# Kernel tuning notes

Measured on AMD Instinct MI355X. Metric: run time of the kernel, lower is better.

## Reference

```python
import jax, jax.numpy as jnp
import numpy as np

B = 16
H, D, DV = 8, 64, 64
MAX_SEQLEN = 1024
ALPHA = 1.0


def setup_inputs() -> dict:
    key = jax.random.key(0)
    lengths = np.array([512 + (b * 97) % 513 for b in range(B)], dtype=np.int32)
    offsets = np.concatenate([[0], np.cumsum(lengths)]).astype(np.int32)  # (B+1,)
    T = int(offsets[-1])  # 12137
    k1, k2, k3 = jax.random.split(key, 3)
    tq = jax.random.normal(k1, (T, H * D), dtype=jnp.float32)
    tk = jax.random.normal(k2, (T, H * D), dtype=jnp.float32)
    tv = jax.random.normal(k3, (T, H * DV), dtype=jnp.float32)
    num_candidates = jnp.full((B,), 32, dtype=jnp.int32)
    num_contextuals = jnp.full((B,), 8, dtype=jnp.int32)
    return {
        "tq": tq, "tk": tk, "tv": tv,
        "offsets": jnp.asarray(offsets),
        "max_seqlen": MAX_SEQLEN,
        "num_candidates": num_candidates,
        "num_contextuals": num_contextuals,
    }


def _valid_attn_mask(N, lengths, num_candidates, num_contextuals):
    # HSTU mask: causal within history, contextual tokens act as position 0
    # (attend/attended bidirectionally w.r.t. history), targets (candidates)
    # attend to all history + themselves only (target_group_size == 1).
    ids = jnp.arange(N, dtype=jnp.int32)[None, :]              # (1, N)
    c = num_contextuals[:, None]                                # (B, 1)
    ids_adj = jnp.maximum(ids - c + 1, 0)                       # (B, N)
    max_ids = (lengths - num_contextuals + 1 - num_candidates)[:, None]  # (B, 1)
    ids_adj = jnp.minimum(ids_adj, max_ids)                     # all targets share id == max_ids
    row = ids_adj[:, :, None]                                   # (B, N, 1)
    col = ids_adj[:, None, :]                                   # (B, 1, N)
    dist = row - col
    eye = jnp.eye(N, dtype=bool)[None]
    valid = eye | (dist > 0)                                    # causal + self
    # contextual rows (adjusted id 0) attend all history (but not targets)
    valid = valid | ((row == 0) & (col < max_ids[:, :, None]))
    # mask out padding
    pad = jnp.arange(N, dtype=jnp.int32)[None, :] < lengths[:, None]  # (B, N)
    valid = valid & pad[:, :, None] & pad[:, None, :]
    return valid


def reference(tq, tk, tv, offsets, max_seqlen, num_candidates, num_contextuals):
    T = tq.shape[0]
    Bb = offsets.shape[0] - 1
    N = max_seqlen
    lengths = offsets[1:] - offsets[:-1]                        # (B,)
    # jagged -> padded dense via scatter
    t = jnp.arange(T, dtype=jnp.int32)
    b_idx = jnp.searchsorted(offsets, t, side="right").astype(jnp.int32) - 1
    n_idx = t - offsets[b_idx]
    q = jnp.zeros((Bb, N, H, D), tq.dtype).at[b_idx, n_idx].set(tq.reshape(T, H, D))
    k = jnp.zeros((Bb, N, H, D), tk.dtype).at[b_idx, n_idx].set(tk.reshape(T, H, D))
    v = jnp.zeros((Bb, N, H, DV), tv.dtype).at[b_idx, n_idx].set(tv.reshape(T, H, DV))
    valid = _valid_attn_mask(N, lengths, num_candidates, num_contextuals)  # (B, N, N)
    qk = jnp.einsum("bnhd,bmhd->bhnm", q, k) * ALPHA
    # HSTU non-softmax attention: silu(scores) / max_seqlen, masked
    attn = (jax.nn.silu(qk) / N) * valid[:, None, :, :].astype(qk.dtype)
    out = jnp.einsum("bhnm,bmhd->bnhd", attn, v)                # (B, N, H, DV)
    # padded -> jagged gather
    return out[b_idx, n_idx].reshape(T, H * DV)
```

## Files before the change

kernel.cpp:

```cpp
#include <hip/hip_runtime.h>
#include <math.h>


#define HH      8
#define DDIM    64
#define QT      64
#define KT      64
#define STRIDE  512
#define NMAX    1024
#define NORD    16
#define TILE_HW 8192
#define NBLK    1024
#define SLOTS   8

typedef __attribute__((ext_vector_type(8))) short short8;
typedef __attribute__((ext_vector_type(4))) float f32x4;
typedef __attribute__((ext_vector_type(4))) uint  u32x4;

static __device__ __forceinline__ uint pk2(float a, float b) {
  uint r;
  asm("v_cvt_pk_bf16_f32 %0, %1, %2" : "=v"(r) : "v"(a), "v"(b));
  return r;
}

static __device__ __forceinline__ void dma16(const ushort* g, ushort* l) {
  __builtin_amdgcn_global_load_lds(
      (const __attribute__((address_space(1))) void*)g,
      (__attribute__((address_space(3))) void*)l, 16, 0, 0);
}

__global__ void build_tiles(const float* __restrict__ tk,
                            const float* __restrict__ tv,
                            ushort* __restrict__ tiles,
                            const int* __restrict__ offsets,
                            short* __restrict__ sched, int Bb) {
  const int mt = blockIdx.x, h = blockIdx.y, b = blockIdx.z;
  const int off = offsets[b];
  const int L   = offsets[b + 1] - off;
  const int tid = threadIdx.x;
  const bool sched_block = (mt == 0 && h == 0 && b == 0);

  if (mt * 64 < L) {
    ushort* img = tiles + (size_t)((b * NORD + mt) * HH + h) * TILE_HW;
    const int row = tid >> 2;
    const int c0  = (tid & 3) * 16;
    const int m   = mt * 64 + row;
    const int sw  = (row & 7) << 3;

    __shared__ ushort tr[64][66];

    {
      uint u[8];
      if (m < L) {
        const float* s = tk + (size_t)(off + m) * STRIDE + h * DDIM + c0;
        float4 a = *(const float4*)(s),      b4 = *(const float4*)(s + 4);
        float4 c4 = *(const float4*)(s + 8), d4 = *(const float4*)(s + 12);
        u[0] = pk2(a.x, a.y);   u[1] = pk2(a.z, a.w);
        u[2] = pk2(b4.x, b4.y); u[3] = pk2(b4.z, b4.w);
        u[4] = pk2(c4.x, c4.y); u[5] = pk2(c4.z, c4.w);
        u[6] = pk2(d4.x, d4.y); u[7] = pk2(d4.z, d4.w);
      } else {
#pragma unroll
        for (int j = 0; j < 8; ++j) u[j] = 0u;
      }
      *(uint4*)&img[row * 64 + (c0 ^ sw)]       = make_uint4(u[0], u[1], u[2], u[3]);
      *(uint4*)&img[row * 64 + ((c0 + 8) ^ sw)] = make_uint4(u[4], u[5], u[6], u[7]);
    }
    {
      uint u[8];
      if (m < L) {
        const float* s = tv + (size_t)(off + m) * STRIDE + h * DDIM + c0;
        float4 a = *(const float4*)(s),      b4 = *(const float4*)(s + 4);
        float4 c4 = *(const float4*)(s + 8), d4 = *(const float4*)(s + 12);
        u[0] = pk2(a.x, a.y);   u[1] = pk2(a.z, a.w);
        u[2] = pk2(b4.x, b4.y); u[3] = pk2(b4.z, b4.w);
        u[4] = pk2(c4.x, c4.y); u[5] = pk2(c4.z, c4.w);
        u[6] = pk2(d4.x, d4.y); u[7] = pk2(d4.z, d4.w);
      } else {
#pragma unroll
        for (int j = 0; j < 8; ++j) u[j] = 0u;
      }
#pragma unroll
      for (int j = 0; j < 8; ++j) *(uint*)&tr[row][c0 + 2 * j] = u[j];
    }
    __syncthreads();
    {
      uint u[8];
#pragma unroll
      for (int j = 0; j < 8; ++j)
        u[j] = (uint)tr[c0 + 2 * j][row] | ((uint)tr[c0 + 2 * j + 1][row] << 16);
      *(uint4*)&img[4096 + row * 64 + (c0 ^ sw)]       = make_uint4(u[0], u[1], u[2], u[3]);
      *(uint4*)&img[4096 + row * 64 + ((c0 + 8) ^ sw)] = make_uint4(u[4], u[5], u[6], u[7]);
    }
  }

  if (!sched_block) return;
  for (int i = tid; i < NBLK * SLOTS; i += 256) sched[i] = (short)-1;
  __syncthreads();
  if (tid < 64) {
    const int g = tid >> 3, hh = tid & 7;
    int nq[16];
    {
      int o0 = offsets[0];
      for (int bb = 0; bb < Bb; ++bb) {
        int o1 = offsets[bb + 1];
        nq[bb] = (o1 - o0 + QT - 1) / QT;
        o0 = o1;
      }
    }
    int gb0 = -1, gb1 = -1;
    for (int bb = 0; bb < Bb; ++bb) {
      int r = 0;
      for (int j = 0; j < Bb; ++j)
        r += (nq[j] > nq[bb]) || (nq[j] == nq[bb] && j < bb);
      int gg = (r < Bb / 2) ? (r & 7) : ((Bb - 1 - r) & 7);
      if (gg == g) { if (r < Bb / 2) gb0 = bb; else gb1 = bb; }
    }
    int i = 0;
    for (int cst = 16; cst >= 1; --cst) {
      for (int s = 0; s < 2; ++s) {
        int bb = (s == 0) ? gb0 : gb1;
        if (bb < 0) continue;
        const int q = nq[bb];
        for (int which = 0; which < 2; ++which) {
          int qt = -1;
          if (which == 0 && cst == q) qt = 0;
          if (which == 1 && cst <= q && cst >= 2) qt = cst - 1;
          if (qt < 0) continue;
          const int rank = i * 8 + hh;
          const int pos  = rank & 255;
          const int lb   = (pos < 128) ? pos : 255 - pos;
          const int blk  = g + 8 * lb;
          const int slot = (pos < 128) ? 2 * (rank >> 8) : 2 * (rank >> 8) + 1;
          if (slot < SLOTS)
            sched[blk * SLOTS + slot] = (short)((bb << 7) | (hh << 4) | qt);
          ++i;
        }
      }
    }
  }
}

__global__ void zero_ctr(uint* ctr) { *ctr = 0u; }

__launch_bounds__(256, 4)
__global__ void hstu_s(const float* __restrict__ tq,
                       const ushort* __restrict__ tiles,
                       const short* __restrict__ sched,
                       const int* __restrict__ offsets,
                       const int* __restrict__ pN,
                       const int* __restrict__ ncand,
                       const int* __restrict__ nctx,
                       float* __restrict__ out, int Tm1) {
  __shared__ ushort KV[2][TILE_HW];
  __shared__ ushort Ps[4 * 1024];

  const int tid  = threadIdx.x;
  const int w    = tid >> 6;
  const int lane = tid & 63;
  const int lo   = lane & 15;
  const int hi   = lane >> 4;

  const float invN = 1.0f / (float)pN[0];
  ushort* Pw = &Ps[w * 1024];
  const short* my = sched + blockIdx.x * SLOTS;

  for (int slot = 0; slot < SLOTS; ++slot) {
    const int e = my[slot];
    if (e < 0) return;
    const int b = (e >> 7) & 15, h = (e >> 4) & 7, qt = e & 15;
    const int off = offsets[b];
    const int L   = offsets[b + 1] - off;
    const int n0  = qt * QT;
    if (n0 >= L) continue;

    const int c = nctx[b];
    const int M = L - c + 1 - ncand[b];
    const int m_hi  = (n0 < c) ? L : min(n0 + QT, L);
    const int niter = (m_hi + KT - 1) / KT;

    const ushort* ibase = tiles + (size_t)(b * NORD * HH + h) * TILE_HW;

    __syncthreads();

    {
      const ushort* src = ibase + w * 2048 + lane * 8;
      ushort* dst = &KV[0][w * 2048];
#pragma unroll
      for (int i = 0; i < 4; ++i) dma16(src + i * 512, dst + i * 512);
    }

    short8 qf[2];
    {
      int qr = min(off + n0 + w * 16 + lo, Tm1);
      const float* qp = tq + (size_t)qr * STRIDE + h * DDIM + hi * 8;
      float4 qa = *(const float4*)(qp);
      float4 qb = *(const float4*)(qp + 4);
      float4 qc = *(const float4*)(qp + 32);
      float4 qd = *(const float4*)(qp + 36);
      u32x4 v0 = {pk2(qa.x, qa.y), pk2(qa.z, qa.w), pk2(qb.x, qb.y), pk2(qb.z, qb.w)};
      u32x4 v1 = {pk2(qc.x, qc.y), pk2(qc.z, qc.w), pk2(qd.x, qd.y), pk2(qd.z, qd.w)};
      qf[0] = __builtin_bit_cast(short8, v0);
      qf[1] = __builtin_bit_cast(short8, v1);
    }

    const int  n   = n0 + w * 16 + lo;
    const int  an  = min(max(n - c + 1, 0), M);
    const int  thr = (an > 0 ? an : M) + c - 1;
    const bool nok = n < L;

    f32x4 oacc[4];
#pragma unroll
    for (int i = 0; i < 4; ++i) oacc[i] = (f32x4){0.f, 0.f, 0.f, 0.f};

    for (int t = 0; t < niter; ++t) {
      __syncthreads();

      if (t + 1 < niter) {
        const ushort* src = ibase + (size_t)(t + 1) * (HH * TILE_HW)
                            + w * 2048 + lane * 8;
        ushort* dst = &KV[(t + 1) & 1][w * 2048];
#pragma unroll
        for (int i = 0; i < 4; ++i) dma16(src + i * 512, dst + i * 512);
      }

      const ushort* Kb = KV[t & 1];
      const ushort* Vb = Kb + 4096;
      const int m0 = t * KT;

#pragma unroll
      for (int kc = 0; kc < 4; ++kc) {
        const int krw = kc * 16 + lo;
        const int ksw = (krw & 7) << 3;
        short8 kf0 = *(const short8*)&Kb[krw * 64 + ((hi * 8) ^ ksw)];
        short8 kf1 = *(const short8*)&Kb[krw * 64 + ((32 + hi * 8) ^ ksw)];
        f32x4 s4 = (f32x4){0.f, 0.f, 0.f, 0.f};
        s4 = __builtin_amdgcn_mfma_f32_16x16x32_bf16(kf0, qf[0], s4, 0, 0, 0);
        s4 = __builtin_amdgcn_mfma_f32_16x16x32_bf16(kf1, qf[1], s4, 0, 0, 0);
        const int mb = m0 + kc * 16 + 4 * hi;
        float pp[4];
#pragma unroll
        for (int r = 0; r < 4; ++r) {
          const int mm = mb + r;
          const bool valid = nok & ((mm < thr) | (mm == n));
          float s = valid ? s4[r] : 0.f;
          pp[r] = s * invN * __builtin_amdgcn_rcpf(1.f + __expf(-s));
        }
        const int col = kc * 16 + 4 * hi;
        *(uint2*)&Pw[lo * 64 + (col ^ ((lo & 7) << 3))] =
            make_uint2(pk2(pp[0], pp[1]), pk2(pp[2], pp[3]));
      }

#pragma unroll
      for (int mc = 0; mc < 2; ++mc) {
        short8 pf = *(const short8*)&Pw[lo * 64 + ((mc * 32 + hi * 8) ^ ((lo & 7) << 3))];
#pragma unroll
        for (int dvc = 0; dvc < 4; ++dvc) {
          const int vrow = dvc * 16 + lo;
          short8 vf = *(const short8*)&Vb[vrow * 64 + ((mc * 32 + hi * 8) ^ ((vrow & 7) << 3))];
          oacc[dvc] = __builtin_amdgcn_mfma_f32_16x16x32_bf16(pf, vf, oacc[dvc], 0, 0, 0);
        }
      }
    }

#pragma unroll
    for (int dvc = 0; dvc < 4; ++dvc) {
#pragma unroll
      for (int r = 0; r < 4; ++r) {
        int nn = n0 + w * 16 + hi * 4 + r;
        if (nn < L)
          out[(size_t)(off + nn) * STRIDE + h * DDIM + dvc * 16 + lo] = oacc[dvc][r];
      }
    }
  }
}

__launch_bounds__(256)
__global__ void hstu_fb(const float* __restrict__ tq,
                        const float* __restrict__ tk,
                        const float* __restrict__ tv,
                        const int* __restrict__ offsets,
                        const int* __restrict__ pN,
                        const int* __restrict__ ncand,
                        const int* __restrict__ nctx,
                        float* __restrict__ out,
                        uint* __restrict__ ctr,
                        int Tm1, int Bb) {
  const int bhc    = Bb * HH;
  const int nitems = NORD * bhc;

  __shared__ ushort Ks[KT * DDIM];
  __shared__ ushort Vt[DDIM * KT];
  __shared__ ushort Ps[4 * 1024];
  __shared__ int s_item;

  const int tid  = threadIdx.x;
  const int w    = tid >> 6;
  const int lane = tid & 63;
  const int lo   = lane & 15;
  const int hi   = lane >> 4;
  const float invN = 1.0f / (float)pN[0];
  ushort* Pw = &Ps[w * 1024];

  for (;;) {
    __syncthreads();
    if (tid == 0) s_item = (int)atomicAdd(ctr, 1u);
    __syncthreads();
    const int item = s_item;
    if (item >= nitems) return;
    const int ord = item / bhc;
    const int rem = item - ord * bhc;
    const int b = rem / HH, h = rem - b * HH;
    const int qt = (ord == 0) ? 0 : (NORD - ord);
    const int off = offsets[b];
    const int L   = offsets[b + 1] - off;
    const int n0  = qt * QT;
    if (n0 >= L) continue;

    const int c = nctx[b];
    const int M = L - c + 1 - ncand[b];
    const int m_hi  = (n0 < c) ? L : min(n0 + QT, L);
    const int niter = (m_hi + KT - 1) / KT;

    short8 qf[2];
    {
      int qr = min(off + n0 + w * 16 + lo, Tm1);
      const float* qp = tq + (size_t)qr * STRIDE + h * DDIM + hi * 8;
      float4 qa = *(const float4*)(qp);
      float4 qb = *(const float4*)(qp + 4);
      float4 qc = *(const float4*)(qp + 32);
      float4 qd = *(const float4*)(qp + 36);
      u32x4 v0 = {pk2(qa.x, qa.y), pk2(qa.z, qa.w), pk2(qb.x, qb.y), pk2(qb.z, qb.w)};
      u32x4 v1 = {pk2(qc.x, qc.y), pk2(qc.z, qc.w), pk2(qd.x, qd.y), pk2(qd.z, qd.w)};
      qf[0] = __builtin_bit_cast(short8, v0);
      qf[1] = __builtin_bit_cast(short8, v1);
    }

    const int  n   = n0 + w * 16 + lo;
    const int  an  = min(max(n - c + 1, 0), M);
    const int  thr = (an > 0 ? an : M) + c - 1;
    const bool nok = n < L;

    f32x4 oacc[4];
#pragma unroll
    for (int i = 0; i < 4; ++i) oacc[i] = (f32x4){0.f, 0.f, 0.f, 0.f};

    for (int t = 0; t < niter; ++t) {
      const int m0 = t * KT;
      __syncthreads();
#pragma unroll
      for (int jj = 0; jj < 4; ++jj) {
        int row = (tid >> 4) + jj * 16;
        int r2  = min(off + m0 + row, Tm1);
        float4 kv = *(const float4*)(tk + (size_t)r2 * STRIDE + h * DDIM + (tid & 15) * 4);
        uint2 pk;
        pk.x = pk2(kv.x, kv.y);
        pk.y = pk2(kv.z, kv.w);
        *(uint2*)&Ks[row * 64 + (((tid & 15) * 4) ^ ((row & 7) << 3))] = pk;
      }
      {
        uint bb[8];
#pragma unroll
        for (int j = 0; j < 8; ++j) {
          int ra = min(off + m0 + w * 16 + 2 * j,     Tm1);
          int rb = min(off + m0 + w * 16 + 2 * j + 1, Tm1);
          float va = tv[(size_t)ra * STRIDE + h * DDIM + lane];
          float vb = tv[(size_t)rb * STRIDE + h * DDIM + lane];
          bb[j] = pk2(va, vb);
        }
        int s = (lane & 7) << 3;
        *(uint4*)&Vt[lane * 64 + ((w * 16)     ^ s)] = make_uint4(bb[0], bb[1], bb[2], bb[3]);
        *(uint4*)&Vt[lane * 64 + ((w * 16 + 8) ^ s)] = make_uint4(bb[4], bb[5], bb[6], bb[7]);
      }
      __syncthreads();

#pragma unroll
      for (int kc = 0; kc < 4; ++kc) {
        const int krw = kc * 16 + lo;
        const int ksw = (krw & 7) << 3;
        short8 kf0 = *(const short8*)&Ks[krw * 64 + ((hi * 8) ^ ksw)];
        short8 kf1 = *(const short8*)&Ks[krw * 64 + ((32 + hi * 8) ^ ksw)];
        f32x4 s4 = (f32x4){0.f, 0.f, 0.f, 0.f};
        s4 = __builtin_amdgcn_mfma_f32_16x16x32_bf16(kf0, qf[0], s4, 0, 0, 0);
        s4 = __builtin_amdgcn_mfma_f32_16x16x32_bf16(kf1, qf[1], s4, 0, 0, 0);
        const int mb = m0 + kc * 16 + 4 * hi;
        float pp[4];
#pragma unroll
        for (int r = 0; r < 4; ++r) {
          const int mm = mb + r;
          const bool valid = nok & ((mm < thr) | (mm == n));
          float s = valid ? s4[r] : 0.f;
          pp[r] = s * invN * __builtin_amdgcn_rcpf(1.f + __expf(-s));
        }
        const int col = kc * 16 + 4 * hi;
        *(uint2*)&Pw[lo * 64 + (col ^ ((lo & 7) << 3))] =
            make_uint2(pk2(pp[0], pp[1]), pk2(pp[2], pp[3]));
      }

#pragma unroll
      for (int mc = 0; mc < 2; ++mc) {
        short8 pf = *(const short8*)&Pw[lo * 64 + ((mc * 32 + hi * 8) ^ ((lo & 7) << 3))];
#pragma unroll
        for (int dvc = 0; dvc < 4; ++dvc) {
          const int vrow = dvc * 16 + lo;
          short8 vf = *(const short8*)&Vt[vrow * 64 + ((mc * 32 + hi * 8) ^ ((vrow & 7) << 3))];
          oacc[dvc] = __builtin_amdgcn_mfma_f32_16x16x32_bf16(pf, vf, oacc[dvc], 0, 0, 0);
        }
      }
    }

#pragma unroll
    for (int dvc = 0; dvc < 4; ++dvc) {
#pragma unroll
      for (int r = 0; r < 4; ++r) {
        int nn = n0 + w * 16 + hi * 4 + r;
        if (nn < L)
          out[(size_t)(off + nn) * STRIDE + h * DDIM + dvc * 16 + lo] = oacc[dvc][r];
      }
    }
  }
}

extern "C" void kernel_launch(void* const* d_in, const int* in_sizes, int n_in,
                              void* d_out, int out_size, void* d_ws, size_t ws_size,
                              hipStream_t stream) {
  const float* tq      = (const float*)d_in[0];
  const float* tk      = (const float*)d_in[1];
  const float* tv      = (const float*)d_in[2];
  const int*   offsets = (const int*)d_in[3];
  const int*   pN      = (const int*)d_in[4];
  const int*   ncand   = (const int*)d_in[5];
  const int*   nctx    = (const int*)d_in[6];
  float*       out     = (float*)d_out;

  const int B = in_sizes[3] - 1;
  const int T = in_sizes[0] / STRIDE;

  uint*   ctr   = (uint*)d_ws;
  short*  sched = (short*)((char*)d_ws + 256);
  ushort* tiles = (ushort*)((char*)d_ws + 256 + NBLK * SLOTS * sizeof(short));
  const size_t need = 256 + NBLK * SLOTS * sizeof(short)
                      + (size_t)B * NORD * HH * TILE_HW * sizeof(ushort);

  dim3 block(256);

  if (ws_size >= need && B <= 16) {
    dim3 tgrid(NORD, HH, B);
    build_tiles<<<tgrid, block, 0, stream>>>(tk, tv, tiles, offsets, sched, B);
    hstu_s<<<NBLK, block, 0, stream>>>(tq, tiles, sched, offsets, pN, ncand,
                                       nctx, out, T - 1);
  } else {
    zero_ctr<<<1, 1, 0, stream>>>(ctr);
    hstu_fb<<<NBLK, block, 0, stream>>>(tq, tk, tv, offsets, pN, ncand,
                                        nctx, out, ctr, T - 1, B);
  }
}
```

Before: 65.02 us.

## Replace pre-swizzled K/V tile images with row-major bf16 K and transposed V

The prep kernel now writes K as jagged row-major bf16 and V as a transposed bf16 matrix indexed by (head, dim) rows and padded batch positions, instead of contiguous swizzled 64x64 tile images. The attention kernel gathers each K/V tile with strided 16-byte LDS DMAs and applies the XOR swizzle on the LDS side through the lane column offset. This shrinks the workspace and drops the zero-padded tiles, at the cost of less contiguous global reads in the main loop. K rows past the sequence end are no longer zero-filled, so K reads for the tail can pick up neighbouring data or unwritten workspace, which relies on masking downstream.

```diff
diff --git a/kernel.cpp b/kernel.cpp
--- a/kernel.cpp
+++ b/kernel.cpp
@@ -29,68 +29,63 @@
       (__attribute__((address_space(3))) void*)l, 16, 0, 0);
 }
 
-__global__ void build_tiles(const float* __restrict__ tk,
-                            const float* __restrict__ tv,
-                            ushort* __restrict__ tiles,
-                            const int* __restrict__ offsets,
-                            short* __restrict__ sched, int Bb) {
+__global__ void prep(const float* __restrict__ tk,
+                     const float* __restrict__ tv,
+                     ushort* __restrict__ kbf,
+                     ushort* __restrict__ vbfT,
+                     const int* __restrict__ offsets,
+                     short* __restrict__ sched, int Bb) {
   const int mt = blockIdx.x, h = blockIdx.y, b = blockIdx.z;
   const int off = offsets[b];
   const int L   = offsets[b + 1] - off;
   const int tid = threadIdx.x;
+  const int VTROW = Bb * NMAX;
   const bool sched_block = (mt == 0 && h == 0 && b == 0);
 
+  __shared__ ushort tr[64][66];
+
   if (mt * 64 < L) {
-    ushort* img = tiles + (size_t)((b * NORD + mt) * HH + h) * TILE_HW;
     const int row = tid >> 2;
     const int c0  = (tid & 3) * 16;
     const int m   = mt * 64 + row;
-    const int sw  = (row & 7) << 3;
-
-    __shared__ ushort tr[64][66];
-
-    {
+    const int mcl = min(m, L - 1);
+
+    if (m < L) {
+      const float* s = tk + (size_t)(off + m) * STRIDE + h * DDIM + c0;
+      float4 a = *(const float4*)(s),      b4 = *(const float4*)(s + 4);
+      float4 c4 = *(const float4*)(s + 8), d4 = *(const float4*)(s + 12);
       uint u[8];
-      if (m < L) {
-        const float* s = tk + (size_t)(off + m) * STRIDE + h * DDIM + c0;
-        float4 a = *(const float4*)(s),      b4 = *(const float4*)(s + 4);
-        float4 c4 = *(const float4*)(s + 8), d4 = *(const float4*)(s + 12);
-        u[0] = pk2(a.x, a.y);   u[1] = pk2(a.z, a.w);
-        u[2] = pk2(b4.x, b4.y); u[3] = pk2(b4.z, b4.w);
-        u[4] = pk2(c4.x, c4.y); u[5] = pk2(c4.z, c4.w);
-        u[6] = pk2(d4.x, d4.y); u[7] = pk2(d4.z, d4.w);
-      } else {
-#pragma unroll
-        for (int j = 0; j < 8; ++j) u[j] = 0u;
-      }
-      *(uint4*)&img[row * 64 + (c0 ^ sw)]       = make_uint4(u[0], u[1], u[2], u[3]);
-      *(uint4*)&img[row * 64 + ((c0 + 8) ^ sw)] = make_uint4(u[4], u[5], u[6], u[7]);
-    }
-    {
+      u[0] = pk2(a.x, a.y);   u[1] = pk2(a.z, a.w);
+      u[2] = pk2(b4.x, b4.y); u[3] = pk2(b4.z, b4.w);
+      u[4] = pk2(c4.x, c4.y); u[5] = pk2(c4.z, c4.w);
+      u[6] = pk2(d4.x, d4.y); u[7] = pk2(d4.z, d4.w);
+      ushort* o = kbf + (size_t)(off + m) * STRIDE + h * DDIM + c0;
+      *(uint4*)(o)     = make_uint4(u[0], u[1], u[2], u[3]);
+      *(uint4*)(o + 8) = make_uint4(u[4], u[5], u[6], u[7]);
+    }
+    {
+      const float* s = tv + (size_t)(off + mcl) * STRIDE + h * DDIM + c0;
+      float4 a = *(const float4*)(s),      b4 = *(const float4*)(s + 4);
+      float4 c4 = *(const float4*)(s + 8), d4 = *(const float4*)(s + 12);
       uint u[8];
-      if (m < L) {
-        const float* s = tv + (size_t)(off + m) * STRIDE + h * DDIM + c0;
-        float4 a = *(const float4*)(s),      b4 = *(const float4*)(s + 4);
-        float4 c4 = *(const float4*)(s + 8), d4 = *(const float4*)(s + 12);
-        u[0] = pk2(a.x, a.y);   u[1] = pk2(a.z, a.w);
-        u[2] = pk2(b4.x, b4.y); u[3] = pk2(b4.z, b4.w);
-        u[4] = pk2(c4.x, c4.y); u[5] = pk2(c4.z, c4.w);
-        u[6] = pk2(d4.x, d4.y); u[7] = pk2(d4.z, d4.w);
-      } else {
-#pragma unroll
-        for (int j = 0; j < 8; ++j) u[j] = 0u;
-      }
+      u[0] = pk2(a.x, a.y);   u[1] = pk2(a.z, a.w);
+      u[2] = pk2(b4.x, b4.y); u[3] = pk2(b4.z, b4.w);
+      u[4] = pk2(c4.x, c4.y); u[5] = pk2(c4.z, c4.w);
+      u[6] = pk2(d4.x, d4.y); u[7] = pk2(d4.z, d4.w);
 #pragma unroll
       for (int j = 0; j < 8; ++j) *(uint*)&tr[row][c0 + 2 * j] = u[j];
     }
     __syncthreads();
     {
-      uint u[8];
+      const int dv = tid >> 2;
+      const int tc = (tid & 3) * 16;
+      uint o[8];
 #pragma unroll
       for (int j = 0; j < 8; ++j)
-        u[j] = (uint)tr[c0 + 2 * j][row] | ((uint)tr[c0 + 2 * j + 1][row] << 16);
-      *(uint4*)&img[4096 + row * 64 + (c0 ^ sw)]       = make_uint4(u[0], u[1], u[2], u[3]);
-      *(uint4*)&img[4096 + row * 64 + ((c0 + 8) ^ sw)] = make_uint4(u[4], u[5], u[6], u[7]);
+        o[j] = (uint)tr[tc + 2 * j][dv] | ((uint)tr[tc + 2 * j + 1][dv] << 16);
+      ushort* orow = vbfT + (size_t)(h * DDIM + dv) * VTROW + b * NMAX + mt * 64 + tc;
+      *(uint4*)(orow)     = make_uint4(o[0], o[1], o[2], o[3]);
+      *(uint4*)(orow + 8) = make_uint4(o[4], o[5], o[6], o[7]);
     }
   }
 
@@ -145,13 +140,14 @@
 
 __launch_bounds__(256, 4)
 __global__ void hstu_s(const float* __restrict__ tq,
-                       const ushort* __restrict__ tiles,
+                       const ushort* __restrict__ kbf,
+                       const ushort* __restrict__ vbfT,
                        const short* __restrict__ sched,
                        const int* __restrict__ offsets,
                        const int* __restrict__ pN,
                        const int* __restrict__ ncand,
                        const int* __restrict__ nctx,
-                       float* __restrict__ out, int Tm1) {
+                       float* __restrict__ out, int Tm1, int Bb) {
   __shared__ ushort KV[2][TILE_HW];
   __shared__ ushort Ps[4 * 1024];
 
@@ -160,6 +156,10 @@
   const int lane = tid & 63;
   const int lo   = lane & 15;
   const int hi   = lane >> 4;
+  const int VTROW = Bb * NMAX;
+
+  const int lr  = lane >> 3;
+  const int csw = ((lane & 7) ^ lr) * 8;
 
   const float invN = 1.0f / (float)pN[0];
   ushort* Pw = &Ps[w * 1024];
@@ -179,15 +179,19 @@
     const int m_hi  = (n0 < c) ? L : min(n0 + QT, L);
     const int niter = (m_hi + KT - 1) / KT;
 
-    const ushort* ibase = tiles + (size_t)(b * NORD * HH + h) * TILE_HW;
+    const ushort* pK = kbf + (size_t)(off + w * 16 + lr) * STRIDE + h * DDIM + csw;
+    const ushort* pV = vbfT + (size_t)(h * DDIM + w * 16 + lr) * VTROW
+                       + (size_t)b * NMAX + csw;
 
     __syncthreads();
 
     {
-      const ushort* src = ibase + w * 2048 + lane * 8;
-      ushort* dst = &KV[0][w * 2048];
-#pragma unroll
-      for (int i = 0; i < 4; ++i) dma16(src + i * 512, dst + i * 512);
+      ushort* dK = &KV[0][w * 1024];
+      ushort* dV = &KV[0][4096 + w * 1024];
+      dma16(pK,                    dK);
+      dma16(pK + 8 * STRIDE,       dK + 512);
+      dma16(pV,                    dV);
+      dma16(pV + (size_t)8 * VTROW, dV + 512);
     }
 
     short8 qf[2];
@@ -217,11 +221,14 @@
       __syncthreads();
 
       if (t + 1 < niter) {
-        const ushort* src = ibase + (size_t)(t + 1) * (HH * TILE_HW)
-                            + w * 2048 + lane * 8;
-        ushort* dst = &KV[(t + 1) & 1][w * 2048];
-#pragma unroll
-        for (int i = 0; i < 4; ++i) dma16(src + i * 512, dst + i * 512);
+        const ushort* sk = pK + (size_t)(t + 1) * (KT * STRIDE);
+        const ushort* sv = pV + (t + 1) * KT;
+        ushort* dK = &KV[(t + 1) & 1][w * 1024];
+        ushort* dV = &KV[(t + 1) & 1][4096 + w * 1024];
+        dma16(sk,                    dK);
+        dma16(sk + 8 * STRIDE,       dK + 512);
+        dma16(sv,                    dV);
+        dma16(sv + (size_t)8 * VTROW, dV + 512);
       }
 
       const ushort* Kb = KV[t & 1];
@@ -436,19 +443,21 @@
   const int B = in_sizes[3] - 1;
   const int T = in_sizes[0] / STRIDE;
 
-  uint*   ctr   = (uint*)d_ws;
-  short*  sched = (short*)((char*)d_ws + 256);
-  ushort* tiles = (ushort*)((char*)d_ws + 256 + NBLK * SLOTS * sizeof(short));
-  const size_t need = 256 + NBLK * SLOTS * sizeof(short)
-                      + (size_t)B * NORD * HH * TILE_HW * sizeof(ushort);
+  uint*   ctr    = (uint*)d_ws;
+  short*  sched  = (short*)((char*)d_ws + 256);
+  ushort* kbf    = (ushort*)((char*)d_ws + 256 + NBLK * SLOTS * sizeof(short));
+  size_t  kbytes = (size_t)T * STRIDE * sizeof(ushort);
+  ushort* vbfT   = (ushort*)((char*)kbf + kbytes);
+  size_t  vbytes = (size_t)STRIDE * (size_t)B * NMAX * sizeof(ushort);
+  const size_t need = 256 + NBLK * SLOTS * sizeof(short) + kbytes + vbytes;
 
   dim3 block(256);
 
   if (ws_size >= need && B <= 16) {
-    dim3 tgrid(NORD, HH, B);
-    build_tiles<<<tgrid, block, 0, stream>>>(tk, tv, tiles, offsets, sched, B);
-    hstu_s<<<NBLK, block, 0, stream>>>(tq, tiles, sched, offsets, pN, ncand,
-                                       nctx, out, T - 1);
+    dim3 pgrid(NORD, HH, B);
+    prep<<<pgrid, block, 0, stream>>>(tk, tv, kbf, vbfT, offsets, sched, B);
+    hstu_s<<<NBLK, block, 0, stream>>>(tq, kbf, vbfT, sched, offsets, pN,
+                                       ncand, nctx, out, T - 1, B);
   } else {
     zero_ctr<<<1, 1, 0, stream>>>(ctr);
     hstu_fb<<<NBLK, block, 0, stream>>>(tq, tk, tv, offsets, pN, ncand,
```

After: 66.65 us. +2.5%, slower.

## Fold 1/N into V tiles and rebalance schedule with greedy per-block load assignment

Applied to the files above, without the earlier changes.

The 1/max_seqlen scale is moved out of the inner attention loop and folded into V during bf16 tile packing, which saves one multiply per score element. The static round-robin scheduler is replaced by a greedy longest-first assignment that gives each work item to the least-loaded of 16 blocks per (group, head), and slots per block grow from 8 to 10. The V transpose indexing is also rewritten. The greedy scheduler runs serially on one block and may cluster work differently, and scaling V before the bf16 cast slightly changes rounding.

```diff
diff --git a/kernel.cpp b/kernel.cpp
--- a/kernel.cpp
+++ b/kernel.cpp
@@ -11,7 +11,7 @@
 #define NORD    16
 #define TILE_HW 8192
 #define NBLK    1024
-#define SLOTS   8
+#define SLOTS   10
 
 typedef __attribute__((ext_vector_type(8))) short short8;
 typedef __attribute__((ext_vector_type(4))) float f32x4;
@@ -33,12 +33,16 @@
                             const float* __restrict__ tv,
                             ushort* __restrict__ tiles,
                             const int* __restrict__ offsets,
+                            const int* __restrict__ pN,
                             short* __restrict__ sched, int Bb) {
   const int mt = blockIdx.x, h = blockIdx.y, b = blockIdx.z;
   const int off = offsets[b];
   const int L   = offsets[b + 1] - off;
   const int tid = threadIdx.x;
+  const float invN = 1.0f / (float)pN[0];
   const bool sched_block = (mt == 0 && h == 0 && b == 0);
+
+  __shared__ ushort tr[64][66];
 
   if (mt * 64 < L) {
     ushort* img = tiles + (size_t)((b * NORD + mt) * HH + h) * TILE_HW;
@@ -46,8 +50,6 @@
     const int c0  = (tid & 3) * 16;
     const int m   = mt * 64 + row;
     const int sw  = (row & 7) << 3;
-
-    __shared__ ushort tr[64][66];
 
     {
       uint u[8];
@@ -72,10 +74,10 @@
         const float* s = tv + (size_t)(off + m) * STRIDE + h * DDIM + c0;
         float4 a = *(const float4*)(s),      b4 = *(const float4*)(s + 4);
         float4 c4 = *(const float4*)(s + 8), d4 = *(const float4*)(s + 12);
-        u[0] = pk2(a.x, a.y);   u[1] = pk2(a.z, a.w);
-        u[2] = pk2(b4.x, b4.y); u[3] = pk2(b4.z, b4.w);
-        u[4] = pk2(c4.x, c4.y); u[5] = pk2(c4.z, c4.w);
-        u[6] = pk2(d4.x, d4.y); u[7] = pk2(d4.z, d4.w);
+        u[0] = pk2(a.x * invN, a.y * invN);   u[1] = pk2(a.z * invN, a.w * invN);
+        u[2] = pk2(b4.x * invN, b4.y * invN); u[3] = pk2(b4.z * invN, b4.w * invN);
+        u[4] = pk2(c4.x * invN, c4.y * invN); u[5] = pk2(c4.z * invN, c4.w * invN);
+        u[6] = pk2(d4.x * invN, d4.y * invN); u[7] = pk2(d4.z * invN, d4.w * invN);
       } else {
 #pragma unroll
         for (int j = 0; j < 8; ++j) u[j] = 0u;
@@ -85,10 +87,12 @@
     }
     __syncthreads();
     {
+      const int dv = tid >> 2;
+      const int tc = (tid & 3) * 16;
       uint u[8];
 #pragma unroll
       for (int j = 0; j < 8; ++j)
-        u[j] = (uint)tr[c0 + 2 * j][row] | ((uint)tr[c0 + 2 * j + 1][row] << 16);
+        u[j] = (uint)tr[tc + 2 * j][dv] | ((uint)tr[tc + 2 * j + 1][dv] << 16);
       *(uint4*)&img[4096 + row * 64 + (c0 ^ sw)]       = make_uint4(u[0], u[1], u[2], u[3]);
       *(uint4*)&img[4096 + row * 64 + ((c0 + 8) ^ sw)] = make_uint4(u[4], u[5], u[6], u[7]);
     }
@@ -116,25 +120,25 @@
       int gg = (r < Bb / 2) ? (r & 7) : ((Bb - 1 - r) & 7);
       if (gg == g) { if (r < Bb / 2) gb0 = bb; else gb1 = bb; }
     }
-    int i = 0;
+    int loads[16], scnt[16];
+    for (int j = 0; j < 16; ++j) { loads[j] = 0; scnt[j] = 0; }
     for (int cst = 16; cst >= 1; --cst) {
       for (int s = 0; s < 2; ++s) {
-        int bb = (s == 0) ? gb0 : gb1;
+        const int bb = (s == 0) ? gb0 : gb1;
         if (bb < 0) continue;
         const int q = nq[bb];
         for (int which = 0; which < 2; ++which) {
           int qt = -1;
           if (which == 0 && cst == q) qt = 0;
-          if (which == 1 && cst <= q && cst >= 2) qt = cst - 1;
+          if (which == 1 && cst >= 2 && cst <= q) qt = cst - 1;
           if (qt < 0) continue;
-          const int rank = i * 8 + hh;
-          const int pos  = rank & 255;
-          const int lb   = (pos < 128) ? pos : 255 - pos;
-          const int blk  = g + 8 * lb;
-          const int slot = (pos < 128) ? 2 * (rank >> 8) : 2 * (rank >> 8) + 1;
-          if (slot < SLOTS)
-            sched[blk * SLOTS + slot] = (short)((bb << 7) | (hh << 4) | qt);
-          ++i;
+          int bj = -1;
+          for (int j = 0; j < 16; ++j)
+            if (scnt[j] < SLOTS && (bj < 0 || loads[j] < loads[bj])) bj = j;
+          loads[bj] += cst;
+          const int blk = g + 8 * (hh * 16 + bj);
+          sched[blk * SLOTS + scnt[bj]] = (short)((bb << 7) | (hh << 4) | qt);
+          scnt[bj]++;
         }
       }
     }
@@ -148,7 +152,6 @@
                        const ushort* __restrict__ tiles,
                        const short* __restrict__ sched,
                        const int* __restrict__ offsets,
-                       const int* __restrict__ pN,
                        const int* __restrict__ ncand,
                        const int* __restrict__ nctx,
                        float* __restrict__ out, int Tm1) {
@@ -161,7 +164,6 @@
   const int lo   = lane & 15;
   const int hi   = lane >> 4;
 
-  const float invN = 1.0f / (float)pN[0];
   ushort* Pw = &Ps[w * 1024];
   const short* my = sched + blockIdx.x * SLOTS;
 
@@ -244,7 +246,7 @@
           const int mm = mb + r;
           const bool valid = nok & ((mm < thr) | (mm == n));
           float s = valid ? s4[r] : 0.f;
-          pp[r] = s * invN * __builtin_amdgcn_rcpf(1.f + __expf(-s));
+          pp[r] = s * __builtin_amdgcn_rcpf(1.f + __expf(-s));
         }
         const int col = kc * 16 + 4 * hi;
         *(uint2*)&Pw[lo * 64 + (col ^ ((lo & 7) << 3))] =
@@ -446,8 +448,8 @@
 
   if (ws_size >= need && B <= 16) {
     dim3 tgrid(NORD, HH, B);
-    build_tiles<<<tgrid, block, 0, stream>>>(tk, tv, tiles, offsets, sched, B);
-    hstu_s<<<NBLK, block, 0, stream>>>(tq, tiles, sched, offsets, pN, ncand,
+    build_tiles<<<tgrid, block, 0, stream>>>(tk, tv, tiles, offsets, pN, sched, B);
+    hstu_s<<<NBLK, block, 0, stream>>>(tq, tiles, sched, offsets, ncand,
                                        nctx, out, T - 1);
   } else {
     zero_ctr<<<1, 1, 0, stream>>>(ctr);
```

Result: slower. 145.6 us (+123.9%).
